# Performance work log

Measured on AMD Instinct MI355X. Metric: run time of the kernel, lower is better.

## Reference

```python
import jax, jax.numpy as jnp
import numpy as np

N_NODES = 50000
N_EDGES = 800000
IN_F, HID_F, OUT_F = 512, 128, 16


def setup_inputs() -> dict:
    key = jax.random.key(0)
    k1, k2, k3, k4, k5, k6 = jax.random.split(key, 6)
    x = jax.random.normal(k1, (N_NODES, IN_F), dtype=jnp.float32)
    edge_src = jax.random.randint(k2, (N_EDGES,), 0, N_NODES, dtype=jnp.int32)
    edge_dst = jax.random.randint(k3, (N_EDGES,), 0, N_NODES, dtype=jnp.int32)
    edge_val = jax.random.uniform(k4, (N_EDGES,), dtype=jnp.float32)
    # Xavier uniform init like torch.nn.init.xavier_uniform_
    lim1 = float(np.sqrt(6.0 / (IN_F + HID_F)))
    lim2 = float(np.sqrt(6.0 / (HID_F + OUT_F)))
    W1 = jax.random.uniform(k5, (IN_F, HID_F), minval=-lim1, maxval=lim1, dtype=jnp.float32)
    W2 = jax.random.uniform(k6, (HID_F, OUT_F), minval=-lim2, maxval=lim2, dtype=jnp.float32)
    return {"x": x, "edge_src": edge_src, "edge_dst": edge_dst, "edge_val": edge_val, "W1": W1, "W2": W2}


def _spmm(edge_val, edge_src, edge_dst, dense, n_nodes):
    # out[i] = sum_{e: dst(e)=i} val(e) * dense[src(e)]  == sparse_adj @ dense
    gathered = edge_val[:, None] * dense[edge_src]  # [E, F]
    return jax.ops.segment_sum(gathered, edge_dst, num_segments=n_nodes)


def reference(x, edge_src, edge_dst, edge_val, W1, W2):
    n = x.shape[0]
    # layer 1: mm -> spmm -> relu
    h = jax.nn.relu(_spmm(edge_val, edge_src, edge_dst, x @ W1, n))
    # dropout(p=0.5) is identity in eval mode (training=False)
    # layer 2: mm -> spmm (no relu)
    logits = _spmm(edge_val, edge_src, edge_dst, h @ W2, n)
    return jax.nn.log_softmax(logits, axis=1)
```

## Files before the change

### kernel.cpp

```cpp
#include <hip/hip_runtime.h>
#include <hip/hip_fp16.h>

#define N_NODES 50000
#define N_EDGES 800000
#define IN_F    512
#define HID_F   128
#define OUT_F   16
#define CAP     64

typedef __attribute__((ext_vector_type(8))) short short8v;
typedef __attribute__((ext_vector_type(4))) float float4v;
typedef unsigned int uint32;
typedef unsigned short ushort16;

typedef __attribute__((address_space(3))) void lds_vp;
typedef __attribute__((address_space(1))) const void g_vp;

__device__ __forceinline__ ushort16 f2bf(float f) {
    uint32 u = __float_as_uint(f);
    uint32 r = (u + 0x7FFFu + ((u >> 16) & 1u)) >> 16;
    return (ushort16)r;
}
__device__ __forceinline__ float bf_lo(uint32 h) { return __uint_as_float(h << 16); }
__device__ __forceinline__ float bf_hi(uint32 h) { return __uint_as_float(h & 0xFFFF0000u); }
__device__ __forceinline__ uint32 pack2bf(float a, float b) {
    return (uint32)f2bf(a) | ((uint32)f2bf(b) << 16);
}
__device__ __forceinline__ float pk_val(uint32 u) {
    return __half2float(__ushort_as_half((unsigned short)(u >> 16)));
}

__global__ __launch_bounds__(256) void zero_i(int* __restrict__ p, int n) {
    const int i = blockIdx.x * 256 + threadIdx.x;
    if (i < n) p[i] = 0;
}

__global__ __launch_bounds__(256) void fill_bucket(const int* __restrict__ src,
                                                   const int* __restrict__ dst,
                                                   const float* __restrict__ val,
                                                   int* __restrict__ cursor,
                                                   uint32* __restrict__ bucket) {
    const int e = blockIdx.x * 256 + threadIdx.x;
    if (e >= N_EDGES) return;
    const int d = dst[e];
    const int s = src[e];
    const float v = val[e];
    const int p = atomicAdd(&cursor[d], 1);
    const unsigned short hb = __half_as_ushort(__float2half_rn(v));
    const uint32 pk = (uint32)s | ((uint32)hb << 16);
    if (p < CAP) bucket[(size_t)d * CAP + p] = pk;
}

__global__ __launch_bounds__(256) void w1t_prep(const float* __restrict__ W1,
                                                unsigned short* __restrict__ W1T) {
    const int idx = blockIdx.x * 256 + threadIdx.x;
    if (idx >= IN_F * HID_F) return;
    const int k = idx >> 7;
    const int c = idx & 127;
    W1T[(size_t)c * IN_F + k] = (unsigned short)f2bf(W1[idx]);
}

__global__ __launch_bounds__(256) void gemm1_lds(const float* __restrict__ X,
                                                 const short* __restrict__ W1T,
                                                 ushort16* __restrict__ H0) {
    __shared__ float4  Xs[1024];
    __shared__ short8v Ws[1024];
    const int t    = threadIdx.x;
    const int lane = t & 63;
    const int w    = t >> 6;
    const int l15  = lane & 15;
    const int kg   = (lane >> 4) * 8;
    const int bm   = blockIdx.x * 64;

    float4v acc[8];
#pragma unroll
    for (int n = 0; n < 8; ++n) acc[n] = (float4v){0.f, 0.f, 0.f, 0.f};

    const int ra = w * 16 + l15;

    for (int k0 = 0; k0 < IN_F; k0 += 64) {
#pragma unroll
        for (int i = 0; i < 4; ++i) {
            const int idx = i * 256 + t;
            const int r   = idx >> 4;
            const int s   = idx & 15;
            const int c4  = s ^ (r & 15);
            const int grow = min(bm + r, N_NODES - 1);
            const float* g = X + (size_t)grow * IN_F + k0 + c4 * 4;
            __builtin_amdgcn_global_load_lds((g_vp*)g, (lds_vp*)&Xs[idx], 16, 0, 0);
        }
#pragma unroll
        for (int i = 0; i < 4; ++i) {
            const int idx = i * 256 + t;
            const int col = idx >> 3;
            const int s   = idx & 7;
            const int gsl = s ^ (col & 7);
            const short* g = W1T + (size_t)col * IN_F + k0 + gsl * 8;
            __builtin_amdgcn_global_load_lds((g_vp*)g, (lds_vp*)&Ws[idx], 16, 0, 0);
        }
        __syncthreads();
#pragma unroll
        for (int ks = 0; ks < 64; ks += 32) {
            const int j0 = (ks + kg) >> 2;
            const float4 a0 = Xs[ra * 16 + ((j0)     ^ (ra & 15))];
            const float4 a1 = Xs[ra * 16 + ((j0 + 1) ^ (ra & 15))];
            short8v af;
            af[0] = (short)f2bf(a0.x); af[1] = (short)f2bf(a0.y);
            af[2] = (short)f2bf(a0.z); af[3] = (short)f2bf(a0.w);
            af[4] = (short)f2bf(a1.x); af[5] = (short)f2bf(a1.y);
            af[6] = (short)f2bf(a1.z); af[7] = (short)f2bf(a1.w);
            const int gb = (ks + kg) >> 3;
#pragma unroll
            for (int n = 0; n < 8; ++n) {
                const int col = n * 16 + l15;
                const short8v bf = Ws[col * 8 + (gb ^ (col & 7))];
                acc[n] = __builtin_amdgcn_mfma_f32_16x16x32_bf16(af, bf, acc[n], 0, 0, 0);
            }
        }
        __syncthreads();
    }

    const int crow0 = bm + w * 16 + (lane >> 4) * 4;
#pragma unroll
    for (int rr = 0; rr < 4; ++rr) {
        const int grow = crow0 + rr;
        if (grow < N_NODES) {
#pragma unroll
            for (int n = 0; n < 8; ++n)
                H0[(size_t)grow * HID_F + n * 16 + l15] = f2bf(acc[n][rr]);
        }
    }
}

__global__ __launch_bounds__(256) void spmm1_bucket(const uint32* __restrict__ H0u,
                                                    const int* __restrict__ cursor,
                                                    const uint32* __restrict__ bucket,
                                                    uint32* __restrict__ S1) {
    const int r    = blockIdx.x * 4 + (threadIdx.x >> 6);
    const int lane = threadIdx.x & 63;
    if (r >= N_NODES) return;
    const int cnt = min(cursor[r], CAP);
    const uint32 pk = bucket[(size_t)r * CAP + lane];
    float a0 = 0.f, a1 = 0.f;
    int j = 0;
    for (; j + 8 <= cnt; j += 8) {
        uint32 uu[8], hh[8];
#pragma unroll
        for (int q = 0; q < 8; ++q) {
            uu[q] = __shfl(pk, j + q);
            hh[q] = H0u[(size_t)(uu[q] & 0xFFFF) * 64 + lane];
        }
#pragma unroll
        for (int q = 0; q < 8; ++q) {
            const float v = pk_val(uu[q]);
            a0 += v * bf_lo(hh[q]);
            a1 += v * bf_hi(hh[q]);
        }
    }
    for (; j < cnt; ++j) {
        const uint32 u = __shfl(pk, j);
        const uint32 h = H0u[(size_t)(u & 0xFFFF) * 64 + lane];
        const float v  = pk_val(u);
        a0 += v * bf_lo(h);
        a1 += v * bf_hi(h);
    }
    S1[(size_t)r * 64 + lane] = pack2bf(fmaxf(a0, 0.f), fmaxf(a1, 0.f));
}

__global__ __launch_bounds__(256) void gemm2(const uint32* __restrict__ S1,
                                             const float* __restrict__ W2,
                                             float* __restrict__ H2) {
    __shared__ float w[HID_F * OUT_F];
    const int t = threadIdx.x;
#pragma unroll
    for (int i = 0; i < 8; ++i) w[t + i * 256] = W2[t + i * 256];
    __syncthreads();
    const int c    = t & 15;
    const int rloc = t >> 4;
    const int r    = blockIdx.x * 16 + rloc;
    if (r >= N_NODES) return;
    const uint32* row = S1 + (size_t)r * 64;
    float acc = 0.f;
#pragma unroll 8
    for (int k2 = 0; k2 < 64; ++k2) {
        const uint32 h = row[k2];
        acc += bf_lo(h) * w[(2 * k2) * OUT_F + c];
        acc += bf_hi(h) * w[(2 * k2 + 1) * OUT_F + c];
    }
    H2[(size_t)r * OUT_F + c] = acc;
}

__global__ __launch_bounds__(256) void spmm2_ls(const float* __restrict__ H2,
                                                const int* __restrict__ cursor,
                                                const uint32* __restrict__ bucket,
                                                float* __restrict__ out) {
    const int r = blockIdx.x * 16 + (threadIdx.x >> 4);
    const int f = threadIdx.x & 15;
    if (r >= N_NODES) return;
    const int cnt = min(cursor[r], CAP);
    float acc = 0.f;
    for (int base = 0; base < cnt; base += 16) {
        const uint32 pk = bucket[(size_t)r * CAP + base + f];
        const int lim = min(16, cnt - base);
        int j = 0;
        for (; j + 8 <= lim; j += 8) {
            uint32 uu[8];
            float  hh[8];
#pragma unroll
            for (int q = 0; q < 8; ++q) {
                uu[q] = __shfl(pk, j + q, 16);
                hh[q] = H2[(size_t)(uu[q] & 0xFFFF) * OUT_F + f];
            }
#pragma unroll
            for (int q = 0; q < 8; ++q) acc += pk_val(uu[q]) * hh[q];
        }
        for (; j < lim; ++j) {
            const uint32 u = __shfl(pk, j, 16);
            acc += pk_val(u) * H2[(size_t)(u & 0xFFFF) * OUT_F + f];
        }
    }
    float m = acc;
#pragma unroll
    for (int off = 1; off < 16; off <<= 1) m = fmaxf(m, __shfl_xor(m, off, 16));
    const float ex = __expf(acc - m);
    float ss = ex;
#pragma unroll
    for (int off = 1; off < 16; off <<= 1) ss += __shfl_xor(ss, off, 16);
    out[(size_t)r * OUT_F + f] = acc - m - logf(ss);
}

extern "C" void kernel_launch(void* const* d_in, const int* in_sizes, int n_in,
                              void* d_out, int out_size, void* d_ws, size_t ws_size,
                              hipStream_t stream) {
    const float* x        = (const float*)d_in[0];
    const int*   edge_src = (const int*)d_in[1];
    const int*   edge_dst = (const int*)d_in[2];
    const float* edge_val = (const float*)d_in[3];
    const float* W1       = (const float*)d_in[4];
    const float* W2       = (const float*)d_in[5];
    float* out = (float*)d_out;

    char* ws = (char*)d_ws;
    size_t off = 0;
    ushort16* H0  = (ushort16*)(ws + off); off += (size_t)N_NODES * HID_F * 2;
    uint32* S1    = (uint32*)  (ws + off); off += (size_t)N_NODES * HID_F * 2;
    uint32* bucket= (uint32*)  (ws + off); off += (size_t)N_NODES * CAP * 4;
    int*   cursor = (int*)     (ws + off); off += (size_t)N_NODES * 4;
    unsigned short* W1T = (unsigned short*)(ws + off); off += (size_t)IN_F * HID_F * 2;
    float* H2 = (float*)H0;

    w1t_prep<<<(IN_F * HID_F + 255) / 256, 256, 0, stream>>>(W1, W1T);
    zero_i<<<(N_NODES + 255) / 256, 256, 0, stream>>>(cursor, N_NODES);
    fill_bucket<<<(N_EDGES + 255) / 256, 256, 0, stream>>>(edge_src, edge_dst, edge_val,
                                                           cursor, bucket);

    gemm1_lds<<<(N_NODES + 63) / 64, 256, 0, stream>>>(x, (const short*)W1T, H0);

    spmm1_bucket<<<(N_NODES + 3) / 4, 256, 0, stream>>>((const uint32*)H0, cursor, bucket, S1);

    gemm2<<<(N_NODES + 15) / 16, 256, 0, stream>>>(S1, W2, H2);

    spmm2_ls<<<(N_NODES + 15) / 16, 256, 0, stream>>>(H2, cursor, bucket, out);
}
```

Before: 135.7 us.

## Double-buffer gemm1 LDS tiles, merge prep kernels, unroll spmm1 gathers by 16

The first GEMM now keeps two LDS buffers for its X and W1T tiles. The next K tile is issued with global_load_lds while MFMAs run on the current one, so the load-then-compute pattern with two barriers per tile becomes overlapped. The W1 transpose and cursor-zeroing kernels are merged into one launch to save a launch. The first SpMM gets a 16-wide gather loop to put more independent loads in flight. The costs are doubled LDS use, which may lower occupancy, and higher register pressure in the spmm loop.

```diff
diff --git a/kernel.cpp b/kernel.cpp
--- a/kernel.cpp
+++ b/kernel.cpp
@@ -30,9 +30,16 @@
     return __half2float(__ushort_as_half((unsigned short)(u >> 16)));
 }
 
-__global__ __launch_bounds__(256) void zero_i(int* __restrict__ p, int n) {
-    const int i = blockIdx.x * 256 + threadIdx.x;
-    if (i < n) p[i] = 0;
+__global__ __launch_bounds__(256) void prep(const float* __restrict__ W1,
+                                            unsigned short* __restrict__ W1T,
+                                            int* __restrict__ cursor) {
+    const int idx = blockIdx.x * 256 + threadIdx.x;
+    if (idx < IN_F * HID_F) {
+        const int k = idx >> 7;
+        const int c = idx & 127;
+        W1T[(size_t)c * IN_F + k] = (unsigned short)f2bf(W1[idx]);
+    }
+    if (idx < N_NODES) cursor[idx] = 0;
 }
 
 __global__ __launch_bounds__(256) void fill_bucket(const int* __restrict__ src,
@@ -51,20 +58,11 @@
     if (p < CAP) bucket[(size_t)d * CAP + p] = pk;
 }
 
-__global__ __launch_bounds__(256) void w1t_prep(const float* __restrict__ W1,
-                                                unsigned short* __restrict__ W1T) {
-    const int idx = blockIdx.x * 256 + threadIdx.x;
-    if (idx >= IN_F * HID_F) return;
-    const int k = idx >> 7;
-    const int c = idx & 127;
-    W1T[(size_t)c * IN_F + k] = (unsigned short)f2bf(W1[idx]);
-}
-
 __global__ __launch_bounds__(256) void gemm1_lds(const float* __restrict__ X,
                                                  const short* __restrict__ W1T,
                                                  ushort16* __restrict__ H0) {
-    __shared__ float4  Xs[1024];
-    __shared__ short8v Ws[1024];
+    __shared__ float4  Xs[2][1024];
+    __shared__ short8v Ws[2][1024];
     const int t    = threadIdx.x;
     const int lane = t & 63;
     const int w    = t >> 6;
@@ -78,7 +76,9 @@
 
     const int ra = w * 16 + l15;
 
-    for (int k0 = 0; k0 < IN_F; k0 += 64) {
+    const int xr   = t >> 2;
+    const int xs   = t & 3;
+    auto stage = [&](int b, int k0) {
 #pragma unroll
         for (int i = 0; i < 4; ++i) {
             const int idx = i * 256 + t;
@@ -87,7 +87,7 @@
             const int c4  = s ^ (r & 15);
             const int grow = min(bm + r, N_NODES - 1);
             const float* g = X + (size_t)grow * IN_F + k0 + c4 * 4;
-            __builtin_amdgcn_global_load_lds((g_vp*)g, (lds_vp*)&Xs[idx], 16, 0, 0);
+            __builtin_amdgcn_global_load_lds((g_vp*)g, (lds_vp*)&Xs[b][idx], 16, 0, 0);
         }
 #pragma unroll
         for (int i = 0; i < 4; ++i) {
@@ -96,14 +96,22 @@
             const int s   = idx & 7;
             const int gsl = s ^ (col & 7);
             const short* g = W1T + (size_t)col * IN_F + k0 + gsl * 8;
-            __builtin_amdgcn_global_load_lds((g_vp*)g, (lds_vp*)&Ws[idx], 16, 0, 0);
-        }
-        __syncthreads();
+            __builtin_amdgcn_global_load_lds((g_vp*)g, (lds_vp*)&Ws[b][idx], 16, 0, 0);
+        }
+    };
+
+    stage(0, 0);
+    __syncthreads();
+
+#pragma unroll
+    for (int kt = 0; kt < 8; ++kt) {
+        const int cur = kt & 1;
+        if (kt < 7) stage(cur ^ 1, (kt + 1) * 64);
 #pragma unroll
         for (int ks = 0; ks < 64; ks += 32) {
             const int j0 = (ks + kg) >> 2;
-            const float4 a0 = Xs[ra * 16 + ((j0)     ^ (ra & 15))];
-            const float4 a1 = Xs[ra * 16 + ((j0 + 1) ^ (ra & 15))];
+            const float4 a0 = Xs[cur][ra * 16 + ((j0)     ^ (ra & 15))];
+            const float4 a1 = Xs[cur][ra * 16 + ((j0 + 1) ^ (ra & 15))];
             short8v af;
             af[0] = (short)f2bf(a0.x); af[1] = (short)f2bf(a0.y);
             af[2] = (short)f2bf(a0.z); af[3] = (short)f2bf(a0.w);
@@ -113,7 +121,7 @@
 #pragma unroll
             for (int n = 0; n < 8; ++n) {
                 const int col = n * 16 + l15;
-                const short8v bf = Ws[col * 8 + (gb ^ (col & 7))];
+                const short8v bf = Ws[cur][col * 8 + (gb ^ (col & 7))];
                 acc[n] = __builtin_amdgcn_mfma_f32_16x16x32_bf16(af, bf, acc[n], 0, 0, 0);
             }
         }
@@ -143,6 +151,20 @@
     const uint32 pk = bucket[(size_t)r * CAP + lane];
     float a0 = 0.f, a1 = 0.f;
     int j = 0;
+    for (; j + 16 <= cnt; j += 16) {
+        uint32 uu[16], hh[16];
+#pragma unroll
+        for (int q = 0; q < 16; ++q) {
+            uu[q] = __shfl(pk, j + q);
+            hh[q] = H0u[(size_t)(uu[q] & 0xFFFF) * 64 + lane];
+        }
+#pragma unroll
+        for (int q = 0; q < 16; ++q) {
+            const float v = pk_val(uu[q]);
+            a0 += v * bf_lo(hh[q]);
+            a1 += v * bf_hi(hh[q]);
+        }
+    }
     for (; j + 8 <= cnt; j += 8) {
         uint32 uu[8], hh[8];
 #pragma unroll
@@ -249,8 +271,7 @@
     unsigned short* W1T = (unsigned short*)(ws + off); off += (size_t)IN_F * HID_F * 2;
     float* H2 = (float*)H0;
 
-    w1t_prep<<<(IN_F * HID_F + 255) / 256, 256, 0, stream>>>(W1, W1T);
-    zero_i<<<(N_NODES + 255) / 256, 256, 0, stream>>>(cursor, N_NODES);
+    prep<<<(IN_F * HID_F + 255) / 256, 256, 0, stream>>>(W1, W1T, cursor);
     fill_bucket<<<(N_EDGES + 255) / 256, 256, 0, stream>>>(edge_src, edge_dst, edge_val,
                                                            cursor, bucket);
 
```

Result: no change. 135.9 us (+0.1%).
